# Performance work log

Hardware: AMD Instinct MI355X
Metric: run time of the kernel (lower is better)

## Reference

```python
import jax, jax.numpy as jnp
import numpy as np

N_HEADS = 16
N_KV_HEADS = 4
HEAD_DIM = 128
WINDOW = 512
THETA = 10000.0


def _rotate_half(t):
    h = t.shape[-1] // 2
    return jnp.concatenate([-t[..., h:], t[..., :h]], axis=-1)


def setup_inputs() -> dict:
    key = jax.random.key(0)
    ks = jax.random.split(key, 6)
    B, S, D = 1, 2048, 2048
    sd = 1.0 / np.sqrt(D)
    x = jax.random.normal(ks[0], (B, S, D), dtype=jnp.float32)
    Wq = jax.random.normal(ks[1], (D, N_HEADS * HEAD_DIM), dtype=jnp.float32) * sd
    Wk = jax.random.normal(ks[2], (D, N_KV_HEADS * HEAD_DIM), dtype=jnp.float32) * sd
    Wv = jax.random.normal(ks[3], (D, N_KV_HEADS * HEAD_DIM), dtype=jnp.float32) * sd
    Wo = jax.random.normal(ks[4], (N_HEADS * HEAD_DIM, D), dtype=jnp.float32) * sd
    lam = jnp.full((N_HEADS,), 0.1, dtype=jnp.float32)
    return {"x": x, "Wq": Wq, "Wk": Wk, "Wv": Wv, "Wo": Wo, "lam": lam}


def reference(x, Wq, Wk, Wv, Wo, lam):
    B, S, D = x.shape
    H, Hk, hd = N_HEADS, N_KV_HEADS, HEAD_DIM
    n_rep = H // Hk

    q = (x @ Wq).reshape(B, S, H, hd).transpose(0, 2, 1, 3)   # [B,H,S,hd]
    k = (x @ Wk).reshape(B, S, Hk, hd).transpose(0, 2, 1, 3)  # [B,Hk,S,hd]
    v = (x @ Wv).reshape(B, S, Hk, hd).transpose(0, 2, 1, 3)

    # RoPE (full head_dim rotation, duplicated freqs)
    inv_freq = 1.0 / (THETA ** (jnp.arange(0, hd, 2, dtype=jnp.float32) / hd))
    t = jnp.arange(S, dtype=jnp.float32)
    freqs = jnp.outer(t, inv_freq)                 # [S, hd/2]
    emb = jnp.concatenate([freqs, freqs], axis=-1)  # [S, hd]
    cos, sin = jnp.cos(emb), jnp.sin(emb)
    q = q * cos + _rotate_half(q) * sin
    k = k * cos + _rotate_half(k) * sin

    # GQA: repeat KV heads
    k = jnp.repeat(k, n_rep, axis=1)  # [B,H,S,hd]
    v = jnp.repeat(v, n_rep, axis=1)

    sub = hd // 2
    q1, q2 = q[..., :sub], q[..., sub:]
    k1, k2 = k[..., :sub], k[..., sub:]
    scale = 1.0 / np.sqrt(sub)

    attn1 = jnp.einsum("bhqd,bhkd->bhqk", q1, k1) * scale
    attn2 = jnp.einsum("bhqd,bhkd->bhqk", q2, k2) * scale

    # causal + sliding window mask
    row = jnp.arange(S)[:, None]
    col = jnp.arange(S)[None, :]
    allowed = (col <= row) & (col >= row - WINDOW + 1)  # [S,S]
    neg_inf = jnp.float32(-jnp.inf)
    attn1 = jnp.where(allowed, attn1, neg_inf)
    attn2 = jnp.where(allowed, attn2, neg_inf)

    a1 = jax.nn.softmax(attn1.astype(jnp.float32), axis=-1).astype(x.dtype)
    a2 = jax.nn.softmax(attn2.astype(jnp.float32), axis=-1).astype(x.dtype)

    diff = jax.nn.relu(a1 - lam.reshape(1, H, 1, 1) * a2)
    diff = diff / (diff.sum(axis=-1, keepdims=True) + 1e-6)

    out = jnp.einsum("bhqk,bhkd->bhqd", diff, v)       # [B,H,S,hd]
    out = out.transpose(0, 2, 1, 3).reshape(B, S, H * hd)
    return out @ Wo
```

## Files before the change

### kernel.cpp

```cpp
#include <hip/hip_runtime.h>

typedef unsigned int u32;
typedef unsigned short u16;
typedef __attribute__((ext_vector_type(4))) float f32x4;
typedef __attribute__((ext_vector_type(8))) short s16x8;

#define S_LEN 2048
#define DMODEL 2048
#define NH 16
#define NKV 4
#define HD 128
#define WIN 512
#define QSCALE 0.18033688011112042f

__device__ __forceinline__ u16 f2bf(float f) {
  union { float f; u32 u; } v; v.f = f;
  u32 r = v.u + 0x7FFFu + ((v.u >> 16) & 1u);
  return (u16)(r >> 16);
}
__device__ __forceinline__ float bf2f(u16 h) {
  union { u32 u; float f; } v; v.u = ((u32)h) << 16;
  return v.f;
}

__device__ __forceinline__ void async16(const void* g, void* l) {
  __builtin_amdgcn_global_load_lds((const __attribute__((address_space(1))) void*)g,
                                   (__attribute__((address_space(3))) void*)l, 16, 0, 0);
}


__global__ void k_rope_table(float2* __restrict__ cs) {
  int s = blockIdx.x, d = threadIdx.x;
  float invf = expf(-((float)(2 * d) / (float)HD) * logf(10000.0f));
  float fr = (float)s * invf;
  float sv, cv;
  sincosf(fr, &sv, &cv);
  cs[s * 64 + d] = make_float2(cv, sv);
}

__global__ void k_convert_bf16(const float* __restrict__ src, u16* __restrict__ dst, int n4) {
  int i = blockIdx.x * blockDim.x + threadIdx.x;
  if (i >= n4) return;
  float4 v = ((const float4*)src)[i];
  ushort4 o;
  o.x = f2bf(v.x); o.y = f2bf(v.y); o.z = f2bf(v.z); o.w = f2bf(v.w);
  ((ushort4*)dst)[i] = o;
}

__global__ __launch_bounds__(256) void k_transpose_all(const float* __restrict__ Wq,
                                                       const float* __restrict__ Wk,
                                                       const float* __restrict__ Wv,
                                                       const float* __restrict__ Wo,
                                                       u16* __restrict__ WT,
                                                       u16* __restrict__ WoT) {
  __shared__ float tile[32][33];
  const int bid = blockIdx.x;
  const float* src;
  u16* dst;
  int N, nt, kt;
  if (bid < 4096) {
    src = Wq; dst = WT; N = 2048; nt = bid & 63; kt = bid >> 6;
  } else if (bid < 5120) {
    int i = bid - 4096;
    src = Wk; dst = WT + (size_t)2048 * 2048; N = 512; nt = i & 15; kt = i >> 4;
  } else if (bid < 6144) {
    int i = bid - 5120;
    src = Wv; dst = WT + (size_t)2560 * 2048; N = 512; nt = i & 15; kt = i >> 4;
  } else {
    int i = bid - 6144;
    src = Wo; dst = WoT; N = 2048; nt = i & 63; kt = i >> 6;
  }
  const int tx = threadIdx.x & 31, ty = threadIdx.x >> 5;
  const int n0 = nt * 32, k0 = kt * 32;
#pragma unroll
  for (int i = 0; i < 4; ++i)
    tile[ty + 8 * i][tx] = src[(size_t)(k0 + ty + 8 * i) * N + n0 + tx];
  __syncthreads();
#pragma unroll
  for (int i = 0; i < 4; ++i)
    dst[(size_t)(n0 + ty + 8 * i) * 2048 + k0 + tx] = f2bf(tile[tx][ty + 8 * i]);
}

__global__ void k_rope_apply2(u16* __restrict__ qr, u16* __restrict__ kr,
                              const float2* __restrict__ cs) {
  int i = blockIdx.x * blockDim.x + threadIdx.x;
  int rowg = i >> 6, d = i & 63;
  const bool isq = rowg < NH * S_LEN;
  u16* p = isq ? qr + (size_t)rowg * HD : kr + (size_t)(rowg - NH * S_LEN) * HD;
  const float scale = isq ? QSCALE : 1.0f;
  int s = rowg & (S_LEN - 1);
  float2 c = cs[s * 64 + d];
  float a = bf2f(p[d]), b = bf2f(p[d + 64]);
  p[d]      = f2bf((a * c.x - b * c.y) * scale);
  p[d + 64] = f2bf((b * c.x + a * c.y) * scale);
}


template <int MODE>
__global__ __launch_bounds__(256) void k_gemm(const u16* __restrict__ A, const u16* __restrict__ BT,
                                              float* __restrict__ Cf, int K, int N,
                                              u16* __restrict__ qr, u16* __restrict__ kr,
                                              u16* __restrict__ vt) {
  __shared__ u16 S[2][192 * 64];
  const int t = threadIdx.x;
  const int l = t & 63, w = t >> 6;
  const int lg = l >> 4, ll = l & 15;

  const u32 nwg = gridDim.x * gridDim.y;
  const u32 bid = blockIdx.y * gridDim.x + blockIdx.x;
  const u32 sid = (bid & 7u) * (nwg >> 3) + (bid >> 3);
  const int m0 = (int)(sid % gridDim.x) * 64;
  const int n0 = (int)(sid / gridDim.x) * 128;

  const int wm = (w >> 1) * 32, wn = (w & 1) * 64;

  const u16* gp[6];
  u32 lo[6];
#pragma unroll
  for (int j = 0; j < 6; ++j) {
    u32 u = (u32)t * 16u + (u32)j * 4096u;
    u32 row = u >> 7;
    u32 slot = ((u >> 4) & 7u) ^ (row & 7u);
    lo[j] = u;
    gp[j] = (row < 64 ? A + (size_t)(m0 + (int)row) * K
                      : BT + (size_t)(n0 + (int)(row - 64)) * K) + slot * 8;
  }
  auto stage = [&](int b, int k0) {
#pragma unroll
    for (int j = 0; j < 6; ++j) async16(gp[j] + k0, (char*)S[b] + lo[j]);
  };

  f32x4 acc[2][4];
#pragma unroll
  for (int i = 0; i < 2; ++i)
#pragma unroll
    for (int j = 0; j < 4; ++j) acc[i][j] = (f32x4){0.f, 0.f, 0.f, 0.f};

  stage(0, 0);
  __syncthreads();

  const int nit = K / 64;
#pragma unroll 2
  for (int it = 0; it < nit; ++it) {
    const int cur = it & 1;
    if (it + 1 < nit) stage(cur ^ 1, (it + 1) * 64);

    s16x8 af[2][2], bq[4][2];
#pragma unroll
    for (int mt = 0; mt < 2; ++mt) {
      u32 r = (u32)(wm + mt * 16 + ll);
#pragma unroll
      for (int ks = 0; ks < 2; ++ks)
        af[mt][ks] = *(const s16x8*)((const char*)S[cur] + r * 128u +
                                     ((((u32)(ks * 4 + lg)) ^ (r & 7u)) * 16u));
    }
#pragma unroll
    for (int nt = 0; nt < 4; ++nt) {
      u32 r = (u32)(64 + wn + nt * 16 + ll);
#pragma unroll
      for (int ks = 0; ks < 2; ++ks)
        bq[nt][ks] = *(const s16x8*)((const char*)S[cur] + r * 128u +
                                     ((((u32)(ks * 4 + lg)) ^ (r & 7u)) * 16u));
    }
#pragma unroll
    for (int ks = 0; ks < 2; ++ks)
#pragma unroll
      for (int mt = 0; mt < 2; ++mt)
#pragma unroll
        for (int nt = 0; nt < 4; ++nt)
          acc[mt][nt] = __builtin_amdgcn_mfma_f32_16x16x32_bf16(af[mt][ks], bq[nt][ks],
                                                                acc[mt][nt], 0, 0, 0);
    __syncthreads();
  }

  if (MODE == 1) {
#pragma unroll
    for (int mt = 0; mt < 2; ++mt) {
      int srow = m0 + wm + mt * 16 + lg * 4;
#pragma unroll
      for (int nt = 0; nt < 4; ++nt) {
        int col = n0 + wn + nt * 16 + ll;
        f32x4 a = acc[mt][nt];
#pragma unroll
        for (int j = 0; j < 4; ++j) Cf[(size_t)(srow + j) * N + col] = a[j];
      }
    }
  } else {
#pragma unroll
    for (int nt = 0; nt < 4; ++nt) {
      int cb = n0 + wn + nt * 16;
#pragma unroll
      for (int mt = 0; mt < 2; ++mt) {
        int srow = m0 + wm + mt * 16 + lg * 4;
        f32x4 a = acc[mt][nt];
        if (cb < 2048) {
          int hh = cb >> 7, d = (cb & 127) + ll;
          u16* p = qr + ((size_t)hh * S_LEN) * HD + d;
#pragma unroll
          for (int j = 0; j < 4; ++j) p[(size_t)(srow + j) * HD] = f2bf(a[j]);
        } else if (cb < 2560) {
          int hh = (cb - 2048) >> 7, d = ((cb - 2048) & 127) + ll;
          u16* p = kr + ((size_t)hh * S_LEN) * HD + d;
#pragma unroll
          for (int j = 0; j < 4; ++j) p[(size_t)(srow + j) * HD] = f2bf(a[j]);
        } else {
          int hh = (cb - 2560) >> 7, d = ((cb - 2560) & 127) + ll;
          ushort4 pk;
          pk.x = f2bf(a[0]); pk.y = f2bf(a[1]); pk.z = f2bf(a[2]); pk.w = f2bf(a[3]);
          *(ushort4*)(vt + ((size_t)hh * HD + d) * S_LEN + srow) = pk;
        }
      }
    }
  }
}

__global__ __launch_bounds__(256, 4) void k_attn(const u16* __restrict__ qr,
                                                 const u16* __restrict__ kr,
                                                 const u16* __restrict__ vt,
                                                 const float* __restrict__ lam,
                                                 u16* __restrict__ ao) {
  __shared__ u16 KV[2][8192];
  __shared__ u16 P[4][16 * 40];
  const int t = threadIdx.x;
  const int l = t & 63, w = t >> 6;
  const int lg = l >> 4, ll = l & 15;
  const int h = blockIdx.y;
  const int bq = blockIdx.x * 64;
  const int qs = bq + w * 16;
  const int hk = h >> 2;
  const int row = qs + ll;

  const u16* Qp = qr + ((size_t)h * S_LEN + qs) * HD;
  const u16* Kp = kr + (size_t)hk * S_LEN * HD;
  const u16* Vp = vt + (size_t)hk * HD * S_LEN;

  const int kbeg = (bq >= 512) ? bq - 512 : 0;
  const int nch1 = (bq >= 512) ? 9 : (bq / 64 + 1);
  const int nch2 = nch1 * 2;

  u32 ku1[4], kr1[4], ks1[4];
#pragma unroll
  for (int j = 0; j < 4; ++j) {
    u32 u = (u32)t * 16u + (u32)j * 4096u;
    ku1[j] = u;
    kr1[j] = u >> 8;
    ks1[j] = ((u >> 4) & 15u) ^ (kr1[j] & 7u);
  }
  u32 ku2[2], kr2[2], ks2[2], vu2[2], vd2[2], vk2[2];
#pragma unroll
  for (int j = 0; j < 2; ++j) {
    u32 u = (u32)t * 16u + (u32)j * 4096u;
    ku2[j] = u;
    kr2[j] = u >> 8;
    ks2[j] = ((u >> 4) & 15u) ^ (kr2[j] & 7u);
    u32 r = u >> 7;
    u32 lgc = ((u >> 4) & 7u) ^ (r & 7u);
    vu2[j] = u;
    vd2[j] = 2u * r + (lgc >> 2);
    vk2[j] = (lgc & 3u) * 8u;
  }

  s16x8 qa[4];
#pragma unroll
  for (int i = 0; i < 4; ++i)
    qa[i] = *(const s16x8*)(Qp + (size_t)ll * HD + i * 32 + lg * 8);

  const f32x4 zero = {0.f, 0.f, 0.f, 0.f};
  float z1 = 0.f, z2 = 0.f;

#pragma unroll
  for (int j = 0; j < 4; ++j)
    async16(Kp + (size_t)(kbeg + kr1[j]) * HD + ks1[j] * 8, (char*)KV + ku1[j]);

  for (int tc = 0; tc < nch1; ++tc) {
    __syncthreads();
    if (tc + 1 < nch1) {
      const int cn = kbeg + (tc + 1) * 64;
      char* dst = (char*)KV + (size_t)((tc + 1) & 1) * 16384;
#pragma unroll
      for (int j = 0; j < 4; ++j)
        async16(Kp + (size_t)(cn + kr1[j]) * HD + ks1[j] * 8, dst + ku1[j]);
    }
    const int c = kbeg + tc * 64;
    const bool active = (c + 63 >= qs - (WIN - 1)) && (c <= qs + 15);
    if (active) {
      const u16* Kb = (const u16*)((const char*)KV + (size_t)(tc & 1) * 16384);
      float acc1 = 0.f, acc2 = 0.f;
#pragma unroll
      for (int kt = 0; kt < 4; ++kt) {
        const int kbase = c + kt * 16;
        if (kbase > qs + 15 || kbase + 15 < qs - (WIN - 1)) continue;
        const int kr_ = kt * 16 + ll;
        const u16* kp = Kb + kr_ * 128;
        const u32 sw = (u32)(kr_ & 7);
        s16x8 b0 = *(const s16x8*)(kp + ((lg ^ sw) * 8));
        s16x8 b1 = *(const s16x8*)(kp + (((4 + lg) ^ sw) * 8));
        s16x8 b2 = *(const s16x8*)(kp + (((8 + lg) ^ sw) * 8));
        s16x8 b3 = *(const s16x8*)(kp + (((12 + lg) ^ sw) * 8));
        f32x4 a = __builtin_amdgcn_mfma_f32_16x16x32_bf16(b0, qa[0], zero, 0, 0, 0);
        a = __builtin_amdgcn_mfma_f32_16x16x32_bf16(b1, qa[1], a, 0, 0, 0);
        f32x4 b = __builtin_amdgcn_mfma_f32_16x16x32_bf16(b2, qa[2], zero, 0, 0, 0);
        b = __builtin_amdgcn_mfma_f32_16x16x32_bf16(b3, qa[3], b, 0, 0, 0);
        const bool fullk = (kbase + 15 <= qs) && (kbase >= qs - 496);
        if (!fullk) {
#pragma unroll
          for (int j = 0; j < 4; ++j) {
            int key = kbase + lg * 4 + j;
            bool ok = (key <= row) && (key > row - WIN);
            a[j] = ok ? a[j] : -1e30f;
            b[j] = ok ? b[j] : -1e30f;
          }
        }
#pragma unroll
        for (int j = 0; j < 4; ++j) {
          acc1 += __builtin_amdgcn_exp2f(a[j]);
          acc2 += __builtin_amdgcn_exp2f(b[j]);
        }
      }
      z1 += acc1; z2 += acc2;
    }
  }

  z1 += __shfl_xor(z1, 16, 64); z1 += __shfl_xor(z1, 32, 64);
  z2 += __shfl_xor(z2, 16, 64); z2 += __shfl_xor(z2, 32, 64);
  const float l2z1 = __builtin_amdgcn_logf(z1);
  const float l2z2 = __builtin_amdgcn_logf(z2);
  const float lm = lam[h];

  f32x4 o[8];
#pragma unroll
  for (int dt = 0; dt < 8; ++dt) o[dt] = zero;
  float dsum = 0.f;
  u16* Pw = &P[w][0];

  __syncthreads();
#pragma unroll
  for (int j = 0; j < 2; ++j) {
    async16(Kp + (size_t)(kbeg + kr2[j]) * HD + ks2[j] * 8, (char*)KV + ku2[j]);
    async16(Vp + (size_t)vd2[j] * S_LEN + kbeg + vk2[j], (char*)KV + 8192 + vu2[j]);
  }

  for (int tc = 0; tc < nch2; ++tc) {
    __syncthreads();
    if (tc + 1 < nch2) {
      const int cn = kbeg + (tc + 1) * 32;
      char* dst = (char*)KV + (size_t)((tc + 1) & 1) * 16384;
#pragma unroll
      for (int j = 0; j < 2; ++j) {
        async16(Kp + (size_t)(cn + kr2[j]) * HD + ks2[j] * 8, dst + ku2[j]);
        async16(Vp + (size_t)vd2[j] * S_LEN + cn + vk2[j], dst + 8192 + vu2[j]);
      }
    }
    const int c = kbeg + tc * 32;
    const bool active = (c + 31 >= qs - (WIN - 1)) && (c <= qs + 15);
    if (active) {
      const u16* Kb = (const u16*)((const char*)KV + (size_t)(tc & 1) * 16384);
      const u16* Vb = Kb + 4096;
      const bool full = (c + 31 <= qs) && (c >= qs - 496);
      __builtin_amdgcn_s_setprio(1);
#pragma unroll
      for (int kt = 0; kt < 2; ++kt) {
        const int kr_ = kt * 16 + ll;
        const u16* kp = Kb + kr_ * 128;
        const u32 sw = (u32)(kr_ & 7);
        s16x8 b0 = *(const s16x8*)(kp + ((lg ^ sw) * 8));
        s16x8 b1 = *(const s16x8*)(kp + (((4 + lg) ^ sw) * 8));
        s16x8 b2 = *(const s16x8*)(kp + (((8 + lg) ^ sw) * 8));
        s16x8 b3 = *(const s16x8*)(kp + (((12 + lg) ^ sw) * 8));
        f32x4 a = __builtin_amdgcn_mfma_f32_16x16x32_bf16(b0, qa[0], zero, 0, 0, 0);
        a = __builtin_amdgcn_mfma_f32_16x16x32_bf16(b1, qa[1], a, 0, 0, 0);
        f32x4 b = __builtin_amdgcn_mfma_f32_16x16x32_bf16(b2, qa[2], zero, 0, 0, 0);
        b = __builtin_amdgcn_mfma_f32_16x16x32_bf16(b3, qa[3], b, 0, 0, 0);
        if (!full) {
#pragma unroll
          for (int j = 0; j < 4; ++j) {
            int key = c + kt * 16 + lg * 4 + j;
            bool ok = (key <= row) && (key > row - WIN);
            a[j] = ok ? a[j] : -1e30f;
            b[j] = ok ? b[j] : -1e30f;
          }
        }
        float d4[4];
#pragma unroll
        for (int j = 0; j < 4; ++j) {
          float a1 = __builtin_amdgcn_exp2f(a[j] - l2z1);
          float a2 = __builtin_amdgcn_exp2f(b[j] - l2z2);
          float d = fmaxf(fmaf(-lm, a2, a1), 0.f);
          d4[j] = d;
          dsum += d;
        }
        u32 p01, p23;
        asm("v_cvt_pk_bf16_f32 %0, %1, %2" : "=v"(p01) : "v"(d4[0]), "v"(d4[1]));
        asm("v_cvt_pk_bf16_f32 %0, %1, %2" : "=v"(p23) : "v"(d4[2]), "v"(d4[3]));
        uint2 pk; pk.x = p01; pk.y = p23;
        *(uint2*)(&Pw[ll * 40 + kt * 16 + lg * 4]) = pk;
      }
      s16x8 pf = *(const s16x8*)(&Pw[ll * 40 + lg * 8]);
#pragma unroll
      for (int dt = 0; dt < 8; ++dt) {
        const int d = dt * 16 + ll;
        const u32 r = (u32)(d >> 1);
        const u32 phys = ((u32)((d & 1) * 4 + lg)) ^ (r & 7u);
        s16x8 vf = *(const s16x8*)(Vb + r * 64 + phys * 8);
        o[dt] = __builtin_amdgcn_mfma_f32_16x16x32_bf16(pf, vf, o[dt], 0, 0, 0);
      }
      __builtin_amdgcn_s_setprio(0);
    }
  }

  dsum += __shfl_xor(dsum, 16, 64);
  dsum += __shfl_xor(dsum, 32, 64);
  const float rds = __builtin_amdgcn_rcpf(dsum + 1e-6f);
  float rdsj[4];
#pragma unroll
  for (int j = 0; j < 4; ++j) rdsj[j] = __shfl(rds, lg * 4 + j, 64);

#pragma unroll
  for (int dt = 0; dt < 8; ++dt) {
#pragma unroll
    for (int j = 0; j < 4; ++j) {
      int srow = qs + lg * 4 + j;
      ao[(size_t)srow * DMODEL + h * HD + dt * 16 + ll] = f2bf(o[dt][j] * rdsj[j]);
    }
  }
}


extern "C" void kernel_launch(void* const* d_in, const int* in_sizes, int n_in,
                              void* d_out, int out_size, void* d_ws, size_t ws_size,
                              hipStream_t stream) {
  const float* x = (const float*)d_in[0];
  const float* Wq = (const float*)d_in[1];
  const float* Wk = (const float*)d_in[2];
  const float* Wv = (const float*)d_in[3];
  const float* Wo = (const float*)d_in[4];
  const float* lam = (const float*)d_in[5];
  float* out = (float*)d_out;

  char* ws = (char*)d_ws;
  u16* xb = (u16*)(ws);
  u16* WT = (u16*)(ws + (8u << 20));
  u16* WoT = (u16*)(ws + (20u << 20));
  u16* qr = (u16*)(ws + (28u << 20));
  u16* kr = (u16*)(ws + (36u << 20));
  u16* vt = (u16*)(ws + (38u << 20));
  u16* ao = (u16*)(ws + (40u << 20));
  float2* cs = (float2*)(ws + (48u << 20));

  k_rope_table<<<S_LEN, 64, 0, stream>>>(cs);
  k_convert_bf16<<<4096, 256, 0, stream>>>(x, xb, (S_LEN * DMODEL) / 4);

  k_transpose_all<<<10240, 256, 0, stream>>>(Wq, Wk, Wv, Wo, WT, WoT);

  k_gemm<0><<<dim3(32, 24), 256, 0, stream>>>(xb, WT, nullptr, 2048, 3072, qr, kr, vt);

  k_rope_apply2<<<((NH + NKV) * S_LEN * 64) / 256, 256, 0, stream>>>(qr, kr, cs);

  k_attn<<<dim3(S_LEN / 64, NH), 256, 0, stream>>>(qr, kr, vt, lam, ao);

  k_gemm<1><<<dim3(32, 16), 256, 0, stream>>>(ao, WoT, out, 2048, 2048, nullptr, nullptr, nullptr);
}
```

Measured before the change: 123.9 us.

## Merge prep kernels, fuse Q RoPE into attention, triple-buffer KV loads

Merges the x-to-bf16 conversion into the weight transpose kernel so one launch does both. Moves the Q RoPE rotation and scaling into the attention kernel's Q fragment load, leaving a separate RoPE pass only for K. This removes one read and one write of the large Q tensor. The attention K/V staging grows from a double to a four-slot LDS ring with two chunks prefetched ahead, synchronised with explicit vmcnt waits and raw barriers. The larger LDS footprint and the launch bound lowered from 4 to 2 reduce occupancy.

```diff
diff --git a/kernel.cpp b/kernel.cpp
--- a/kernel.cpp
+++ b/kernel.cpp
@@ -13,6 +13,9 @@
 #define WIN 512
 #define QSCALE 0.18033688011112042f
 
+#define WAIT_VMCNT4 asm volatile("s_waitcnt vmcnt(4)" ::: "memory")
+#define WAIT_VMCNT0 asm volatile("s_waitcnt vmcnt(0)" ::: "memory")
+
 __device__ __forceinline__ u16 f2bf(float f) {
   union { float f; u32 u; } v; v.f = f;
   u32 r = v.u + 0x7FFFu + ((v.u >> 16) & 1u);
@@ -38,36 +41,36 @@
   cs[s * 64 + d] = make_float2(cv, sv);
 }
 
-__global__ void k_convert_bf16(const float* __restrict__ src, u16* __restrict__ dst, int n4) {
-  int i = blockIdx.x * blockDim.x + threadIdx.x;
-  if (i >= n4) return;
-  float4 v = ((const float4*)src)[i];
-  ushort4 o;
-  o.x = f2bf(v.x); o.y = f2bf(v.y); o.z = f2bf(v.z); o.w = f2bf(v.w);
-  ((ushort4*)dst)[i] = o;
-}
-
-__global__ __launch_bounds__(256) void k_transpose_all(const float* __restrict__ Wq,
-                                                       const float* __restrict__ Wk,
-                                                       const float* __restrict__ Wv,
-                                                       const float* __restrict__ Wo,
-                                                       u16* __restrict__ WT,
-                                                       u16* __restrict__ WoT) {
+__global__ __launch_bounds__(256) void k_prep(const float* __restrict__ x, u16* __restrict__ xb,
+                                              const float* __restrict__ Wq,
+                                              const float* __restrict__ Wk,
+                                              const float* __restrict__ Wv,
+                                              const float* __restrict__ Wo,
+                                              u16* __restrict__ WT, u16* __restrict__ WoT) {
   __shared__ float tile[32][33];
   const int bid = blockIdx.x;
+  if (bid < 4096) {
+    int i = bid * 256 + threadIdx.x;
+    float4 v = ((const float4*)x)[i];
+    ushort4 o;
+    o.x = f2bf(v.x); o.y = f2bf(v.y); o.z = f2bf(v.z); o.w = f2bf(v.w);
+    ((ushort4*)xb)[i] = o;
+    return;
+  }
+  const int b = bid - 4096;
   const float* src;
   u16* dst;
   int N, nt, kt;
-  if (bid < 4096) {
-    src = Wq; dst = WT; N = 2048; nt = bid & 63; kt = bid >> 6;
-  } else if (bid < 5120) {
-    int i = bid - 4096;
+  if (b < 4096) {
+    src = Wq; dst = WT; N = 2048; nt = b & 63; kt = b >> 6;
+  } else if (b < 5120) {
+    int i = b - 4096;
     src = Wk; dst = WT + (size_t)2048 * 2048; N = 512; nt = i & 15; kt = i >> 4;
-  } else if (bid < 6144) {
-    int i = bid - 5120;
+  } else if (b < 6144) {
+    int i = b - 5120;
     src = Wv; dst = WT + (size_t)2560 * 2048; N = 512; nt = i & 15; kt = i >> 4;
   } else {
-    int i = bid - 6144;
+    int i = b - 6144;
     src = Wo; dst = WoT; N = 2048; nt = i & 63; kt = i >> 6;
   }
   const int tx = threadIdx.x & 31, ty = threadIdx.x >> 5;
@@ -81,18 +84,15 @@
     dst[(size_t)(n0 + ty + 8 * i) * 2048 + k0 + tx] = f2bf(tile[tx][ty + 8 * i]);
 }
 
-__global__ void k_rope_apply2(u16* __restrict__ qr, u16* __restrict__ kr,
-                              const float2* __restrict__ cs) {
+__global__ void k_rope_k(u16* __restrict__ kr, const float2* __restrict__ cs) {
   int i = blockIdx.x * blockDim.x + threadIdx.x;
   int rowg = i >> 6, d = i & 63;
-  const bool isq = rowg < NH * S_LEN;
-  u16* p = isq ? qr + (size_t)rowg * HD : kr + (size_t)(rowg - NH * S_LEN) * HD;
-  const float scale = isq ? QSCALE : 1.0f;
   int s = rowg & (S_LEN - 1);
   float2 c = cs[s * 64 + d];
+  u16* p = kr + (size_t)rowg * HD;
   float a = bf2f(p[d]), b = bf2f(p[d + 64]);
-  p[d]      = f2bf((a * c.x - b * c.y) * scale);
-  p[d + 64] = f2bf((b * c.x + a * c.y) * scale);
+  p[d]      = f2bf(a * c.x - b * c.y);
+  p[d + 64] = f2bf(b * c.x + a * c.y);
 }
 
 
@@ -214,12 +214,13 @@
   }
 }
 
-__global__ __launch_bounds__(256, 4) void k_attn(const u16* __restrict__ qr,
+__global__ __launch_bounds__(256, 2) void k_attn(const u16* __restrict__ qr,
                                                  const u16* __restrict__ kr,
                                                  const u16* __restrict__ vt,
                                                  const float* __restrict__ lam,
+                                                 const float2* __restrict__ cs,
                                                  u16* __restrict__ ao) {
-  __shared__ u16 KV[2][8192];
+  __shared__ u16 KV[4][8192];
   __shared__ u16 P[4][16 * 40];
   const int t = threadIdx.x;
   const int l = t & 63, w = t >> 6;
@@ -264,27 +265,54 @@
 #pragma unroll
   for (int i = 0; i < 4; ++i)
     qa[i] = *(const s16x8*)(Qp + (size_t)ll * HD + i * 32 + lg * 8);
+  {
+    const float4* cp4 = (const float4*)(cs + (size_t)row * 64);
+#pragma unroll
+    for (int i = 0; i < 2; ++i) {
+      float4 cv[4];
+#pragma unroll
+      for (int jj = 0; jj < 4; ++jj) cv[jj] = cp4[i * 16 + lg * 4 + jj];
+      s16x8 lo = qa[i], hi = qa[i + 2];
+#pragma unroll
+      for (int j = 0; j < 8; ++j) {
+        float cc = (j & 1) ? cv[j >> 1].z : cv[j >> 1].x;
+        float ss = (j & 1) ? cv[j >> 1].w : cv[j >> 1].y;
+        float a = bf2f((u16)lo[j]), b = bf2f((u16)hi[j]);
+        lo[j] = (short)f2bf((a * cc - b * ss) * QSCALE);
+        hi[j] = (short)f2bf((b * cc + a * ss) * QSCALE);
+      }
+      qa[i] = lo; qa[i + 2] = hi;
+    }
+  }
 
   const f32x4 zero = {0.f, 0.f, 0.f, 0.f};
   float z1 = 0.f, z2 = 0.f;
 
-#pragma unroll
-  for (int j = 0; j < 4; ++j)
-    async16(Kp + (size_t)(kbeg + kr1[j]) * HD + ks1[j] * 8, (char*)KV + ku1[j]);
+  {
+#pragma unroll
+    for (int j = 0; j < 4; ++j)
+      async16(Kp + (size_t)(kbeg + kr1[j]) * HD + ks1[j] * 8, (char*)KV + ku1[j]);
+    const int c1 = kbeg + ((nch1 > 1) ? 64 : 0);
+#pragma unroll
+    for (int j = 0; j < 4; ++j)
+      async16(Kp + (size_t)(c1 + kr1[j]) * HD + ks1[j] * 8, (char*)KV + 16384 + ku1[j]);
+  }
 
   for (int tc = 0; tc < nch1; ++tc) {
-    __syncthreads();
-    if (tc + 1 < nch1) {
-      const int cn = kbeg + (tc + 1) * 64;
-      char* dst = (char*)KV + (size_t)((tc + 1) & 1) * 16384;
+    WAIT_VMCNT4;
+    __builtin_amdgcn_s_barrier();
+    {
+      int c2i = tc + 2; if (c2i > nch1 - 1) c2i = nch1 - 1;
+      const int c2 = kbeg + c2i * 64;
+      char* dst = (char*)KV + (size_t)((tc + 2) & 3) * 16384;
 #pragma unroll
       for (int j = 0; j < 4; ++j)
-        async16(Kp + (size_t)(cn + kr1[j]) * HD + ks1[j] * 8, dst + ku1[j]);
+        async16(Kp + (size_t)(c2 + kr1[j]) * HD + ks1[j] * 8, dst + ku1[j]);
     }
     const int c = kbeg + tc * 64;
     const bool active = (c + 63 >= qs - (WIN - 1)) && (c <= qs + 15);
     if (active) {
-      const u16* Kb = (const u16*)((const char*)KV + (size_t)(tc & 1) * 16384);
+      const u16* Kb = (const u16*)((const char*)KV + (size_t)(tc & 3) * 16384);
       float acc1 = 0.f, acc2 = 0.f;
 #pragma unroll
       for (int kt = 0; kt < 4; ++kt) {
@@ -333,28 +361,40 @@
   float dsum = 0.f;
   u16* Pw = &P[w][0];
 
+  WAIT_VMCNT0;
   __syncthreads();
-#pragma unroll
-  for (int j = 0; j < 2; ++j) {
-    async16(Kp + (size_t)(kbeg + kr2[j]) * HD + ks2[j] * 8, (char*)KV + ku2[j]);
-    async16(Vp + (size_t)vd2[j] * S_LEN + kbeg + vk2[j], (char*)KV + 8192 + vu2[j]);
+
+  {
+#pragma unroll
+    for (int j = 0; j < 2; ++j) {
+      async16(Kp + (size_t)(kbeg + kr2[j]) * HD + ks2[j] * 8, (char*)KV + ku2[j]);
+      async16(Vp + (size_t)vd2[j] * S_LEN + kbeg + vk2[j], (char*)KV + 8192 + vu2[j]);
+    }
+    const int c1 = kbeg + ((nch2 > 1) ? 32 : 0);
+#pragma unroll
+    for (int j = 0; j < 2; ++j) {
+      async16(Kp + (size_t)(c1 + kr2[j]) * HD + ks2[j] * 8, (char*)KV + 16384 + ku2[j]);
+      async16(Vp + (size_t)vd2[j] * S_LEN + c1 + vk2[j], (char*)KV + 16384 + 8192 + vu2[j]);
+    }
   }
 
   for (int tc = 0; tc < nch2; ++tc) {
-    __syncthreads();
-    if (tc + 1 < nch2) {
-      const int cn = kbeg + (tc + 1) * 32;
-      char* dst = (char*)KV + (size_t)((tc + 1) & 1) * 16384;
+    WAIT_VMCNT4;
+    __builtin_amdgcn_s_barrier();
+    {
+      int c2i = tc + 2; if (c2i > nch2 - 1) c2i = nch2 - 1;
+      const int c2 = kbeg + c2i * 32;
+      char* dst = (char*)KV + (size_t)((tc + 2) & 3) * 16384;
 #pragma unroll
       for (int j = 0; j < 2; ++j) {
-        async16(Kp + (size_t)(cn + kr2[j]) * HD + ks2[j] * 8, dst + ku2[j]);
-        async16(Vp + (size_t)vd2[j] * S_LEN + cn + vk2[j], dst + 8192 + vu2[j]);
+        async16(Kp + (size_t)(c2 + kr2[j]) * HD + ks2[j] * 8, dst + ku2[j]);
+        async16(Vp + (size_t)vd2[j] * S_LEN + c2 + vk2[j], dst + 8192 + vu2[j]);
       }
     }
     const int c = kbeg + tc * 32;
     const bool active = (c + 31 >= qs - (WIN - 1)) && (c <= qs + 15);
     if (active) {
-      const u16* Kb = (const u16*)((const char*)KV + (size_t)(tc & 1) * 16384);
+      const u16* Kb = (const u16*)((const char*)KV + (size_t)(tc & 3) * 16384);
       const u16* Vb = Kb + 4096;
       const bool full = (c + 31 <= qs) && (c >= qs - 496);
       __builtin_amdgcn_s_setprio(1);
@@ -407,6 +447,7 @@
       __builtin_amdgcn_s_setprio(0);
     }
   }
+  WAIT_VMCNT0;
 
   dsum += __shfl_xor(dsum, 16, 64);
   dsum += __shfl_xor(dsum, 32, 64);
@@ -448,15 +489,13 @@
   float2* cs = (float2*)(ws + (48u << 20));
 
   k_rope_table<<<S_LEN, 64, 0, stream>>>(cs);
-  k_convert_bf16<<<4096, 256, 0, stream>>>(x, xb, (S_LEN * DMODEL) / 4);
-
-  k_transpose_all<<<10240, 256, 0, stream>>>(Wq, Wk, Wv, Wo, WT, WoT);
+  k_prep<<<14336, 256, 0, stream>>>(x, xb, Wq, Wk, Wv, Wo, WT, WoT);
 
   k_gemm<0><<<dim3(32, 24), 256, 0, stream>>>(xb, WT, nullptr, 2048, 3072, qr, kr, vt);
 
-  k_rope_apply2<<<((NH + NKV) * S_LEN * 64) / 256, 256, 0, stream>>>(qr, kr, cs);
-
-  k_attn<<<dim3(S_LEN / 64, NH), 256, 0, stream>>>(qr, kr, vt, lam, ao);
+  k_rope_k<<<(NKV * S_LEN * 64) / 256, 256, 0, stream>>>(kr, cs);
+
+  k_attn<<<dim3(S_LEN / 64, NH), 256, 0, stream>>>(qr, kr, vt, lam, cs, ao);
 
   k_gemm<1><<<dim3(32, 16), 256, 0, stream>>>(ao, WoT, out, 2048, 2048, nullptr, nullptr, nullptr);
 }
```

Result: faster. 120.1 us (-3.1%).
